# Optimization experiments

Measured on AMD Instinct MI355X. Metric: run time of the kernel, lower is better.

## Reference

```python
import jax, jax.numpy as jnp
import numpy as np

HEADS = 16
DIM_HEAD = 64
EXPANSION = 2
WINDOW = 512


def setup_inputs() -> dict:
    key = jax.random.key(0)
    ks = jax.random.split(key, 9)
    b, n, dim_q, dim_kv = 2, 2048, 1024, 1024
    di = HEADS * DIM_HEAD          # 1024
    dm = di * EXPANSION            # 2048
    def w(k, shape, fan_in):
        return jax.random.normal(k, shape, jnp.float32) * (fan_in ** -0.5)
    return {
        "queries_input": jax.random.normal(ks[0], (b, n, dim_q), jnp.float32),
        "key_values_input": jax.random.normal(ks[1], (b, n, dim_kv), jnp.float32),
        "Wq": w(ks[2], (dim_q, di), dim_q),
        "Wk1": w(ks[3], (dim_kv, di), dim_kv),
        "Wv1": w(ks[4], (dim_kv, dm), dim_kv),
        "Wk2": w(ks[5], (dim_kv, dm), dim_kv),
        "Wv2": w(ks[6], (dim_kv, di), dim_kv),
        "Wout": w(ks[7], (di, dim_q), di),
        "attn_sink": jax.random.normal(ks[8], (HEADS,), jnp.float32) * 0.01,
    }


def _split_heads(t):
    # b n (h d) -> b h n d
    b, n, _ = t.shape
    return t.reshape(b, n, HEADS, -1).transpose(0, 2, 1, 3)


def _attend(q, k, v, attn_sink, window):
    scale = DIM_HEAD ** -0.5  # fixed at dim_head**-0.5 in both attends, as in the original
    sim = jnp.einsum('bhid,bhjd->bhij', q * scale, k)
    b, _, n, _ = sim.shape
    idx = jnp.arange(n)
    # faithful to original mask indexing (i==j case): mask where j>i and j-i<=window
    mask = (idx[None, :] > idx[:, None]) & (idx[None, :] - idx[:, None] <= window)
    sim = jnp.where(mask, -jnp.finfo(sim.dtype).max, sim)
    # prepend learned per-head sink logit, softmax, then drop the sink column
    sink_col = jnp.broadcast_to(attn_sink[None, :, None, None], (b, HEADS, n, 1))
    attn = jax.nn.softmax(jnp.concatenate([sink_col, sim], axis=-1), axis=-1)[..., 1:]
    return jnp.einsum('bhij,bhjd->bhid', attn, v)


def reference(queries_input, key_values_input, Wq, Wk1, Wv1, Wk2, Wv2, Wout, attn_sink):
    q = _split_heads(queries_input @ Wq)        # [b,h,n,64]
    k1 = _split_heads(key_values_input @ Wk1)   # [b,h,n,64]
    v1 = _split_heads(key_values_input @ Wv1)   # [b,h,n,128]
    k2 = _split_heads(key_values_input @ Wk2)   # [b,h,n,128]
    v2 = _split_heads(key_values_input @ Wv2)   # [b,h,n,64]
    hiddens = _attend(q, k1, v1, attn_sink, WINDOW)     # [b,h,n,128]
    hiddens = jax.nn.silu(hiddens)                       # implicit MLP activation
    out = _attend(hiddens, k2, v2, attn_sink, WINDOW)    # [b,h,n,64]
    b, _, n, _ = out.shape
    out = out.transpose(0, 2, 1, 3).reshape(b, n, -1)    # merge heads
    return out @ Wout
```

## Files before the change

kernel.cpp:

```cpp
#include <hip/hip_runtime.h>
#include <cstddef>
#include <cstdint>

#define NSEQ 2048
#define NB 2
#define NH 16
#define WINDOW 512

typedef __attribute__((ext_vector_type(8))) short short8;
typedef __attribute__((ext_vector_type(4))) float f32x4;
typedef __attribute__((ext_vector_type(4))) unsigned short ushort4v;

__device__ __forceinline__ unsigned short f2bf(float f) {
    union { float f; unsigned u; } v; v.f = f;
    unsigned r = v.u + 0x7FFFu + ((v.u >> 16) & 1u);
    return (unsigned short)(r >> 16);
}

typedef const __attribute__((address_space(1))) unsigned int* gasp;
typedef __attribute__((address_space(3))) unsigned int* lasp;
__device__ __forceinline__ void gll16(const void* g, void* l) {
    __builtin_amdgcn_global_load_lds((gasp)g, (lasp)l, 16, 0, 0);
}

__device__ __forceinline__ f32x4 mfma16(short8 a, short8 b, f32x4 c) {
    return __builtin_amdgcn_mfma_f32_16x16x32_bf16(a, b, c, 0, 0, 0);
}

__global__ __launch_bounds__(256)
void castk(const float* __restrict__ in, unsigned short* __restrict__ out, int n4) {
    int i = blockIdx.x * 256 + threadIdx.x;
    if (i < n4) {
        float4 v = ((const float4*)in)[i];
        ushort4v o;
        o[0] = f2bf(v.x); o[1] = f2bf(v.y); o[2] = f2bf(v.z); o[3] = f2bf(v.w);
        ((ushort4v*)out)[i] = o;
    }
}

__global__ __launch_bounds__(256)
void wtrans(const float* __restrict__ Wsrc, unsigned short* __restrict__ Wt, int K, int N) {
    __shared__ float tile[32][33];
    const int tx = threadIdx.x, ty = threadIdx.y;
    const int n0 = blockIdx.x * 32, k0 = blockIdx.y * 32;
#pragma unroll
    for (int i = 0; i < 4; ++i)
        tile[ty + i * 8][tx] = Wsrc[(size_t)(k0 + ty + i * 8) * N + n0 + tx];
    __syncthreads();
#pragma unroll
    for (int i = 0; i < 4; ++i)
        Wt[(size_t)(n0 + ty + i * 8) * K + k0 + tx] = f2bf(tile[tx][ty + i * 8]);
}

#define OUT_F32 0
#define OUT_BF16 1
#define OUT_VT 2

template <int OMODE, int DVH>
__global__ __launch_bounds__(256)
void gemm_bf16(const unsigned short* __restrict__ A,
               const unsigned short* __restrict__ Bt,
               void* __restrict__ Cout, int K, int ldc)
{
    __shared__ __align__(16) unsigned short As[128 * 32];
    __shared__ __align__(16) unsigned short Bs[128 * 32];
    const int t = threadIdx.x;
    const int l = t & 63, w = t >> 6;
    const int q = l & 15, g = l >> 4;
    const int bm = blockIdx.y * 128, bn = blockIdx.x * 128;
    const int wm = (w & 1) * 64, wn = (w >> 1) * 64;

    f32x4 acc[4][4];
    const f32x4 zero = {0.f, 0.f, 0.f, 0.f};
#pragma unroll
    for (int i = 0; i < 4; ++i)
#pragma unroll
        for (int j = 0; j < 4; ++j) acc[i][j] = zero;

    const unsigned short* Abase = A + (size_t)bm * K;
    const unsigned short* Bbase = Bt + (size_t)bn * K;

    for (int k0 = 0; k0 < K; k0 += 32) {
        __syncthreads();
#pragma unroll
        for (int it = 0; it < 2; ++it) {
            int c = w * 128 + it * 64 + l;
            int r = c >> 2, sg = c & 3;
            gll16(Abase + (size_t)r * K + k0 + sg * 8, (char*)As + c * 16);
            gll16(Bbase + (size_t)r * K + k0 + sg * 8, (char*)Bs + c * 16);
        }
        __syncthreads();
        short8 a[4], b[4];
#pragma unroll
        for (int ms = 0; ms < 4; ++ms)
            a[ms] = *(const short8*)(As + (wm + ms * 16 + q) * 32 + g * 8);
#pragma unroll
        for (int ns = 0; ns < 4; ++ns)
            b[ns] = *(const short8*)(Bs + (wn + ns * 16 + q) * 32 + g * 8);
#pragma unroll
        for (int ms = 0; ms < 4; ++ms)
#pragma unroll
            for (int ns = 0; ns < 4; ++ns)
                acc[ms][ns] = mfma16(a[ms], b[ns], acc[ms][ns]);
    }

    if constexpr (OMODE == OUT_F32) {
        float* C = (float*)Cout;
#pragma unroll
        for (int ms = 0; ms < 4; ++ms)
#pragma unroll
            for (int r = 0; r < 4; ++r) {
                int row = bm + wm + ms * 16 + g * 4 + r;
                float* crow = C + (size_t)row * ldc + bn + wn;
#pragma unroll
                for (int ns = 0; ns < 4; ++ns) crow[ns * 16 + q] = acc[ms][ns][r];
            }
    } else if constexpr (OMODE == OUT_BF16) {
        unsigned short* C = (unsigned short*)Cout;
#pragma unroll
        for (int ms = 0; ms < 4; ++ms)
#pragma unroll
            for (int r = 0; r < 4; ++r) {
                int row = bm + wm + ms * 16 + g * 4 + r;
                unsigned short* crow = C + (size_t)row * ldc + bn + wn;
#pragma unroll
                for (int ns = 0; ns < 4; ++ns) crow[ns * 16 + q] = f2bf(acc[ms][ns][r]);
            }
    } else {
        unsigned short* C = (unsigned short*)Cout;
#pragma unroll
        for (int ms = 0; ms < 4; ++ms) {
            int row0 = bm + wm + ms * 16 + g * 4;
            int bb = row0 >> 11, nn = row0 & 2047;
#pragma unroll
            for (int ns = 0; ns < 4; ++ns) {
                int col = bn + wn + ns * 16 + q;
                int h = col / DVH, d = col % DVH;
                ushort4v pk;
#pragma unroll
                for (int r = 0; r < 4; ++r) pk[r] = f2bf(acc[ms][ns][r]);
                *(ushort4v*)(C + ((size_t)((bb * NH + h) * DVH + d)) * NSEQ + nn) = pk;
            }
        }
    }
}

template <int DK, int DV, bool SILU, bool Q_PH, bool O_PH>
__global__ __launch_bounds__(256)
void attend_mfma(const unsigned short* __restrict__ Qg,
                 const unsigned short* __restrict__ Kg,
                 const unsigned short* __restrict__ Vtg,
                 const float* __restrict__ sink,
                 unsigned short* __restrict__ Og)
{
    constexpr int KT = 64;
    constexpr int NS = DV / 16;
    constexpr int NDB = DK / 32;
    constexpr int KROWB = DK * 2;
    constexpr int KSEGS = KROWB / 16;

    __shared__ __align__(16) char KsB[64 * DK * 2];
    __shared__ __align__(16) char VtB[DV * 64 * 2];
    __shared__ __align__(16) char PsB[64 * 128];

    const int t = threadIdx.x, l = t & 63, w = t >> 6;
    const int q = l & 15, g = l >> 4;
    const int bh = blockIdx.x, bi = bh >> 4, h = bh & 15;
    const int i0 = blockIdx.y * 64;
    const int iq = i0 + w * 16 + q;
    const int qrow = w * 16 + q;

    const unsigned short* qbase;
    if constexpr (Q_PH)
        qbase = Qg + ((size_t)((bi * NH + h) * NSEQ + iq)) * DK;
    else
        qbase = Qg + ((size_t)(bi * NSEQ + iq)) * (NH * DK) + h * DK;
    short8 qf[NDB];
#pragma unroll
    for (int db = 0; db < NDB; ++db)
        qf[db] = *(const short8*)(qbase + db * 32 + g * 8);

    float m = sink[h], lsum = 1.0f;
    f32x4 o[NS];
    const f32x4 zero = {0.f, 0.f, 0.f, 0.f};
#pragma unroll
    for (int ns = 0; ns < NS; ++ns) o[ns] = zero;

    const unsigned short* kbase = Kg + (size_t)(bi * NSEQ) * (NH * DK) + h * DK;
    const unsigned short* vbase = Vtg + (size_t)((bi * NH + h) * DV) * NSEQ;

    for (int j0 = 0; j0 < NSEQ; j0 += KT) {
        const int dd = j0 - i0;
        if (dd >= KT && dd <= WINDOW - KT) continue;

        __syncthreads();
#pragma unroll
        for (int it = 0; it < (64 * KSEGS) / 256; ++it) {
            int c = w * (64 * KSEGS / 4) + it * 64 + l;
            int kv = c / KSEGS, sgst = c % KSEGS;
            int sgsrc = sgst ^ (kv & 7);
            gll16(kbase + (size_t)(j0 + kv) * (NH * DK) + sgsrc * 8, KsB + c * 16);
        }
#pragma unroll
        for (int it = 0; it < (DV * 8) / 256; ++it) {
            int c = w * (DV * 8 / 4) + it * 64 + l;
            int d = c >> 3, sgst = c & 7;
            int sgsrc = sgst ^ (d & 7);
            gll16(vbase + (size_t)d * NSEQ + j0 + sgsrc * 8, VtB + c * 16);
        }
        __syncthreads();

        float st[4][4];
#pragma unroll
        for (int s = 0; s < 4; ++s) {
            f32x4 sacc = zero;
            int kvr = s * 16 + q;
#pragma unroll
            for (int db = 0; db < NDB; ++db) {
                short8 kf = *(const short8*)(KsB + kvr * KROWB + (((db * 4 + g) ^ (kvr & 7)) << 4));
                sacc = mfma16(kf, qf[db], sacc);
            }
#pragma unroll
            for (int r = 0; r < 4; ++r) st[s][r] = sacc[r];
        }

        float mx = -3.0e38f;
#pragma unroll
        for (int s = 0; s < 4; ++s)
#pragma unroll
            for (int r = 0; r < 4; ++r) {
                int j = j0 + s * 16 + g * 4 + r;
                float v = st[s][r] * 0.125f;
                if (j > iq && (j - iq) <= WINDOW) v = -3.0e38f;
                st[s][r] = v;
                mx = fmaxf(mx, v);
            }
        mx = fmaxf(mx, __shfl_xor(mx, 16));
        mx = fmaxf(mx, __shfl_xor(mx, 32));
        const float nm = fmaxf(m, mx);
        const float corr = __expf(m - nm);
        m = nm;
        float ps = 0.f;
#pragma unroll
        for (int s = 0; s < 4; ++s) {
            ushort4v pk;
#pragma unroll
            for (int r = 0; r < 4; ++r) {
                float p = __expf(st[s][r] - nm);
                ps += p;
                pk[r] = f2bf(p);
            }
            *(ushort4v*)(PsB + qrow * 128 + ((s * 32 + g * 8) ^ ((q & 7) << 4))) = pk;
        }
        ps += __shfl_xor(ps, 16);
        ps += __shfl_xor(ps, 32);
        lsum = lsum * corr + ps;

        float cr[4];
#pragma unroll
        for (int r = 0; r < 4; ++r) cr[r] = __shfl(corr, g * 4 + r);
#pragma unroll
        for (int ns = 0; ns < NS; ++ns)
#pragma unroll
            for (int r = 0; r < 4; ++r) o[ns][r] *= cr[r];

#pragma unroll
        for (int kb = 0; kb < 2; ++kb) {
            short8 pf = *(const short8*)(PsB + qrow * 128 + ((((kb * 4 + g) ^ (q & 7))) << 4));
#pragma unroll
            for (int ns = 0; ns < NS; ++ns) {
                int d = ns * 16 + q;
                short8 vf = *(const short8*)(VtB + d * 128 + (((kb * 4 + g) ^ (d & 7)) << 4));
                o[ns] = mfma16(pf, vf, o[ns]);
            }
        }
    }

    const float inv = 1.0f / lsum;
    float ivr[4];
#pragma unroll
    for (int r = 0; r < 4; ++r) ivr[r] = __shfl(inv, g * 4 + r);
#pragma unroll
    for (int ns = 0; ns < NS; ++ns)
#pragma unroll
        for (int r = 0; r < 4; ++r) {
            float x = o[ns][r] * ivr[r];
            if constexpr (SILU) x = x / (1.0f + __expf(-x));
            int qr = i0 + w * 16 + g * 4 + r;
            int d = ns * 16 + q;
            size_t off;
            if constexpr (O_PH)
                off = ((size_t)((bi * NH + h) * NSEQ + qr)) * DV + d;
            else
                off = ((size_t)(bi * NSEQ + qr)) * (NH * DV) + h * DV + d;
            Og[off] = f2bf(x);
        }
}

extern "C" void kernel_launch(void* const* d_in, const int* in_sizes, int n_in,
                              void* d_out, int out_size, void* d_ws, size_t ws_size,
                              hipStream_t stream)
{
    (void)in_sizes; (void)n_in; (void)out_size; (void)ws_size;
    const float* queries = (const float*)d_in[0];
    const float* kvin    = (const float*)d_in[1];
    const float* Wq      = (const float*)d_in[2];
    const float* Wk1     = (const float*)d_in[3];
    const float* Wv1     = (const float*)d_in[4];
    const float* Wk2     = (const float*)d_in[5];
    const float* Wv2     = (const float*)d_in[6];
    const float* Wout    = (const float*)d_in[7];
    const float* sink    = (const float*)d_in[8];
    float* out = (float*)d_out;

    unsigned short* Xq   = (unsigned short*)d_ws;
    unsigned short* Xkv  = Xq   + (size_t)4096 * 1024;
    unsigned short* Wqt  = Xkv  + (size_t)4096 * 1024;
    unsigned short* Wk1t = Wqt  + (size_t)1024 * 1024;
    unsigned short* Wv1t = Wk1t + (size_t)1024 * 1024;
    unsigned short* Wk2t = Wv1t + (size_t)2048 * 1024;
    unsigned short* Wv2t = Wk2t + (size_t)2048 * 1024;
    unsigned short* Wot  = Wv2t + (size_t)1024 * 1024;
    unsigned short* Qp   = Wot  + (size_t)1024 * 1024;
    unsigned short* K1p  = Qp   + (size_t)4096 * 1024;
    unsigned short* V1t  = K1p  + (size_t)4096 * 1024;
    unsigned short* K2p  = V1t  + (size_t)2 * 16 * 128 * 2048;
    unsigned short* V2t  = K2p  + (size_t)4096 * 2048;
    unsigned short* Hb   = V2t  + (size_t)2 * 16 * 64 * 2048;
    unsigned short* AO   = Hb   + (size_t)2 * 16 * 2048 * 128;

    dim3 blk(256);
    dim3 tblk(32, 8);

    castk<<<4096, blk, 0, stream>>>(queries, Xq, 1048576);
    castk<<<4096, blk, 0, stream>>>(kvin, Xkv, 1048576);
    wtrans<<<dim3(32, 32), tblk, 0, stream>>>(Wq,   Wqt,  1024, 1024);
    wtrans<<<dim3(32, 32), tblk, 0, stream>>>(Wk1,  Wk1t, 1024, 1024);
    wtrans<<<dim3(64, 32), tblk, 0, stream>>>(Wv1,  Wv1t, 1024, 2048);
    wtrans<<<dim3(64, 32), tblk, 0, stream>>>(Wk2,  Wk2t, 1024, 2048);
    wtrans<<<dim3(32, 32), tblk, 0, stream>>>(Wv2,  Wv2t, 1024, 1024);
    wtrans<<<dim3(32, 32), tblk, 0, stream>>>(Wout, Wot,  1024, 1024);

    gemm_bf16<OUT_BF16, 1><<<dim3(8, 32), blk, 0, stream>>>(Xq,  Wqt,  Qp,  1024, 1024);
    gemm_bf16<OUT_BF16, 1><<<dim3(8, 32), blk, 0, stream>>>(Xkv, Wk1t, K1p, 1024, 1024);
    gemm_bf16<OUT_VT, 128><<<dim3(16, 32), blk, 0, stream>>>(Xkv, Wv1t, V1t, 1024, 0);
    gemm_bf16<OUT_BF16, 1><<<dim3(16, 32), blk, 0, stream>>>(Xkv, Wk2t, K2p, 1024, 2048);
    gemm_bf16<OUT_VT, 64><<<dim3(8, 32), blk, 0, stream>>>(Xkv, Wv2t, V2t, 1024, 0);

    attend_mfma<64, 128, true, false, true><<<dim3(32, 32), blk, 0, stream>>>(
        Qp, K1p, V1t, sink, Hb);
    attend_mfma<128, 64, false, true, false><<<dim3(32, 32), blk, 0, stream>>>(
        Hb, K2p, V2t, sink, AO);

    gemm_bf16<OUT_F32, 1><<<dim3(8, 32), blk, 0, stream>>>(AO, Wot, out, 1024, 1024);
}
```

Before: 490.5 us.

## Fold softmax scale into Q projection, use exp2 with lazy rescale, fuse KV GEMMs

The four key/value projection GEMMs are merged into one launch over a concatenated weight matrix. The epilogue routes each column range to K1, V1 (transposed), K2 or V2 (transposed). The attention softmax scale times log2(e) is folded into the Q projection output and into the SiLU output that feeds the second attention, so the kernels can use exp2 without a per-element multiply. Masking now runs only on the two boundary tiles. The running-max rescale of the accumulators is skipped unless the max grows by more than 8 in log2 units. Probabilities are packed to bf16 with a hardware pack-convert instruction. These changes cut ALU and launch overhead, but the fused GEMM depends on the transposed weights being contiguous in the workspace, and the lazy rescale lets unnormalized values grow up to 2^8.

```diff
diff --git a/kernel.cpp b/kernel.cpp
--- a/kernel.cpp
+++ b/kernel.cpp
@@ -7,6 +7,9 @@
 #define NH 16
 #define WINDOW 512
 
+#define LOG2E 1.44269504088896f
+#define QSCALE 0.180336877396f
+
 typedef __attribute__((ext_vector_type(8))) short short8;
 typedef __attribute__((ext_vector_type(4))) float f32x4;
 typedef __attribute__((ext_vector_type(4))) unsigned short ushort4v;
@@ -15,6 +18,12 @@
     union { float f; unsigned u; } v; v.f = f;
     unsigned r = v.u + 0x7FFFu + ((v.u >> 16) & 1u);
     return (unsigned short)(r >> 16);
+}
+
+__device__ __forceinline__ unsigned cvt_pk_bf16(float a, float b) {
+    unsigned r;
+    asm("v_cvt_pk_bf16_f32 %0, %1, %2" : "=v"(r) : "v"(a), "v"(b));
+    return r;
 }
 
 typedef const __attribute__((address_space(1))) unsigned int* gasp;
@@ -54,13 +63,15 @@
 
 #define OUT_F32 0
 #define OUT_BF16 1
-#define OUT_VT 2
-
-template <int OMODE, int DVH>
+#define OUT_KV 2
+
+template <int OMODE>
 __global__ __launch_bounds__(256)
 void gemm_bf16(const unsigned short* __restrict__ A,
                const unsigned short* __restrict__ Bt,
-               void* __restrict__ Cout, int K, int ldc)
+               void* __restrict__ Cout, int K, int ldc, float oscale,
+               unsigned short* __restrict__ K1p, unsigned short* __restrict__ V1t,
+               unsigned short* __restrict__ K2p, unsigned short* __restrict__ V2t)
 {
     __shared__ __align__(16) unsigned short As[128 * 32];
     __shared__ __align__(16) unsigned short Bs[128 * 32];
@@ -113,7 +124,7 @@
                 int row = bm + wm + ms * 16 + g * 4 + r;
                 float* crow = C + (size_t)row * ldc + bn + wn;
 #pragma unroll
-                for (int ns = 0; ns < 4; ++ns) crow[ns * 16 + q] = acc[ms][ns][r];
+                for (int ns = 0; ns < 4; ++ns) crow[ns * 16 + q] = acc[ms][ns][r] * oscale;
             }
     } else if constexpr (OMODE == OUT_BF16) {
         unsigned short* C = (unsigned short*)Cout;
@@ -124,22 +135,59 @@
                 int row = bm + wm + ms * 16 + g * 4 + r;
                 unsigned short* crow = C + (size_t)row * ldc + bn + wn;
 #pragma unroll
-                for (int ns = 0; ns < 4; ++ns) crow[ns * 16 + q] = f2bf(acc[ms][ns][r]);
+                for (int ns = 0; ns < 4; ++ns) crow[ns * 16 + q] = f2bf(acc[ms][ns][r] * oscale);
             }
     } else {
-        unsigned short* C = (unsigned short*)Cout;
-#pragma unroll
-        for (int ms = 0; ms < 4; ++ms) {
-            int row0 = bm + wm + ms * 16 + g * 4;
-            int bb = row0 >> 11, nn = row0 & 2047;
-#pragma unroll
-            for (int ns = 0; ns < 4; ++ns) {
-                int col = bn + wn + ns * 16 + q;
-                int h = col / DVH, d = col % DVH;
-                ushort4v pk;
-#pragma unroll
-                for (int r = 0; r < 4; ++r) pk[r] = f2bf(acc[ms][ns][r]);
-                *(ushort4v*)(C + ((size_t)((bb * NH + h) * DVH + d)) * NSEQ + nn) = pk;
+        const int colbase = bn + wn;
+        if (colbase < 1024) {
+#pragma unroll
+            for (int ms = 0; ms < 4; ++ms)
+#pragma unroll
+                for (int r = 0; r < 4; ++r) {
+                    int row = bm + wm + ms * 16 + g * 4 + r;
+                    unsigned short* crow = K1p + (size_t)row * 1024 + colbase;
+#pragma unroll
+                    for (int ns = 0; ns < 4; ++ns) crow[ns * 16 + q] = f2bf(acc[ms][ns][r]);
+                }
+        } else if (colbase < 3072) {
+#pragma unroll
+            for (int ms = 0; ms < 4; ++ms) {
+                int row0 = bm + wm + ms * 16 + g * 4;
+                int bb = row0 >> 11, nn = row0 & 2047;
+#pragma unroll
+                for (int ns = 0; ns < 4; ++ns) {
+                    int c2 = colbase - 1024 + ns * 16 + q;
+                    int h = c2 >> 7, d = c2 & 127;
+                    ushort4v pk;
+#pragma unroll
+                    for (int r = 0; r < 4; ++r) pk[r] = f2bf(acc[ms][ns][r]);
+                    *(ushort4v*)(V1t + ((size_t)((bb * NH + h) * 128 + d)) * NSEQ + nn) = pk;
+                }
+            }
+        } else if (colbase < 5120) {
+#pragma unroll
+            for (int ms = 0; ms < 4; ++ms)
+#pragma unroll
+                for (int r = 0; r < 4; ++r) {
+                    int row = bm + wm + ms * 16 + g * 4 + r;
+                    unsigned short* crow = K2p + (size_t)row * 2048 + colbase - 3072;
+#pragma unroll
+                    for (int ns = 0; ns < 4; ++ns) crow[ns * 16 + q] = f2bf(acc[ms][ns][r]);
+                }
+        } else {
+#pragma unroll
+            for (int ms = 0; ms < 4; ++ms) {
+                int row0 = bm + wm + ms * 16 + g * 4;
+                int bb = row0 >> 11, nn = row0 & 2047;
+#pragma unroll
+                for (int ns = 0; ns < 4; ++ns) {
+                    int c2 = colbase - 5120 + ns * 16 + q;
+                    int h = c2 >> 6, d = c2 & 63;
+                    ushort4v pk;
+#pragma unroll
+                    for (int r = 0; r < 4; ++r) pk[r] = f2bf(acc[ms][ns][r]);
+                    *(ushort4v*)(V2t + ((size_t)((bb * NH + h) * 64 + d)) * NSEQ + nn) = pk;
+                }
             }
         }
     }
@@ -180,7 +228,7 @@
     for (int db = 0; db < NDB; ++db)
         qf[db] = *(const short8*)(qbase + db * 32 + g * 8);
 
-    float m = sink[h], lsum = 1.0f;
+    float m = sink[h] * LOG2E, lsum = 1.0f;
     f32x4 o[NS];
     const f32x4 zero = {0.f, 0.f, 0.f, 0.f};
 #pragma unroll
@@ -224,45 +272,55 @@
             for (int r = 0; r < 4; ++r) st[s][r] = sacc[r];
         }
 
-        float mx = -3.0e38f;
+        if (dd == 0 || dd == WINDOW) {
+#pragma unroll
+            for (int s = 0; s < 4; ++s)
+#pragma unroll
+                for (int r = 0; r < 4; ++r) {
+                    int j = j0 + s * 16 + g * 4 + r;
+                    if (j > iq && (j - iq) <= WINDOW) st[s][r] = -3.0e38f;
+                }
+        }
+
+        float mx = st[0][0];
 #pragma unroll
         for (int s = 0; s < 4; ++s)
 #pragma unroll
-            for (int r = 0; r < 4; ++r) {
-                int j = j0 + s * 16 + g * 4 + r;
-                float v = st[s][r] * 0.125f;
-                if (j > iq && (j - iq) <= WINDOW) v = -3.0e38f;
-                st[s][r] = v;
-                mx = fmaxf(mx, v);
-            }
+            for (int r = 0; r < 4; ++r)
+                if (s || r) mx = fmaxf(mx, st[s][r]);
         mx = fmaxf(mx, __shfl_xor(mx, 16));
         mx = fmaxf(mx, __shfl_xor(mx, 32));
-        const float nm = fmaxf(m, mx);
-        const float corr = __expf(m - nm);
-        m = nm;
+
+        if (!__all(mx - m <= 8.0f)) {
+            const float nm = fmaxf(m, mx);
+            const float corr = exp2f(m - nm);
+            m = nm;
+            lsum *= corr;
+            float cr[4];
+#pragma unroll
+            for (int r = 0; r < 4; ++r) cr[r] = __shfl(corr, g * 4 + r);
+#pragma unroll
+            for (int ns = 0; ns < NS; ++ns)
+#pragma unroll
+                for (int r = 0; r < 4; ++r) o[ns][r] *= cr[r];
+        }
+
         float ps = 0.f;
 #pragma unroll
         for (int s = 0; s < 4; ++s) {
-            ushort4v pk;
-#pragma unroll
-            for (int r = 0; r < 4; ++r) {
-                float p = __expf(st[s][r] - nm);
-                ps += p;
-                pk[r] = f2bf(p);
-            }
-            *(ushort4v*)(PsB + qrow * 128 + ((s * 32 + g * 8) ^ ((q & 7) << 4))) = pk;
+            float p0 = exp2f(st[s][0] - m);
+            float p1 = exp2f(st[s][1] - m);
+            float p2 = exp2f(st[s][2] - m);
+            float p3 = exp2f(st[s][3] - m);
+            ps += (p0 + p1) + (p2 + p3);
+            uint2 pk;
+            pk.x = cvt_pk_bf16(p0, p1);
+            pk.y = cvt_pk_bf16(p2, p3);
+            *(uint2*)(PsB + qrow * 128 + ((s * 32 + g * 8) ^ ((q & 7) << 4))) = pk;
         }
         ps += __shfl_xor(ps, 16);
         ps += __shfl_xor(ps, 32);
-        lsum = lsum * corr + ps;
-
-        float cr[4];
-#pragma unroll
-        for (int r = 0; r < 4; ++r) cr[r] = __shfl(corr, g * 4 + r);
-#pragma unroll
-        for (int ns = 0; ns < NS; ++ns)
-#pragma unroll
-            for (int r = 0; r < 4; ++r) o[ns][r] *= cr[r];
+        lsum += ps;
 
 #pragma unroll
         for (int kb = 0; kb < 2; ++kb) {
@@ -285,7 +343,7 @@
 #pragma unroll
         for (int r = 0; r < 4; ++r) {
             float x = o[ns][r] * ivr[r];
-            if constexpr (SILU) x = x / (1.0f + __expf(-x));
+            if constexpr (SILU) x = x / (1.0f + __expf(-x)) * QSCALE;
             int qr = i0 + w * 16 + g * 4 + r;
             int d = ns * 16 + q;
             size_t off;
@@ -341,16 +399,16 @@
     wtrans<<<dim3(32, 32), tblk, 0, stream>>>(Wv2,  Wv2t, 1024, 1024);
     wtrans<<<dim3(32, 32), tblk, 0, stream>>>(Wout, Wot,  1024, 1024);
 
-    gemm_bf16<OUT_BF16, 1><<<dim3(8, 32), blk, 0, stream>>>(Xq,  Wqt,  Qp,  1024, 1024);
-    gemm_bf16<OUT_BF16, 1><<<dim3(8, 32), blk, 0, stream>>>(Xkv, Wk1t, K1p, 1024, 1024);
-    gemm_bf16<OUT_VT, 128><<<dim3(16, 32), blk, 0, stream>>>(Xkv, Wv1t, V1t, 1024, 0);
-    gemm_bf16<OUT_BF16, 1><<<dim3(16, 32), blk, 0, stream>>>(Xkv, Wk2t, K2p, 1024, 2048);
-    gemm_bf16<OUT_VT, 64><<<dim3(8, 32), blk, 0, stream>>>(Xkv, Wv2t, V2t, 1024, 0);
+    gemm_bf16<OUT_BF16><<<dim3(8, 32), blk, 0, stream>>>(
+        Xq, Wqt, Qp, 1024, 1024, QSCALE, nullptr, nullptr, nullptr, nullptr);
+    gemm_bf16<OUT_KV><<<dim3(48, 32), blk, 0, stream>>>(
+        Xkv, Wk1t, nullptr, 1024, 0, 1.0f, K1p, V1t, K2p, V2t);
 
     attend_mfma<64, 128, true, false, true><<<dim3(32, 32), blk, 0, stream>>>(
         Qp, K1p, V1t, sink, Hb);
     attend_mfma<128, 64, false, true, false><<<dim3(32, 32), blk, 0, stream>>>(
         Hb, K2p, V2t, sink, AO);
 
-    gemm_bf16<OUT_F32, 1><<<dim3(8, 32), blk, 0, stream>>>(AO, Wot, out, 1024, 1024);
-}
+    gemm_bf16<OUT_F32><<<dim3(8, 32), blk, 0, stream>>>(
+        AO, Wot, out, 1024, 1024, 1.0f, nullptr, nullptr, nullptr, nullptr);
+}
```

Result: faster. 426.2 us (-13.1%).
